# Kernel tuning notes

Hardware: AMD Instinct MI355X
Metric: run time of the kernel (lower is better)

## Reference

```python
import jax, jax.numpy as jnp
import numpy as np

TEMP = 0.5  # init kwarg `tmp`
NUM_CLASSES = 100


def setup_inputs() -> dict:
    key = jax.random.key(0)
    k1, k2 = jax.random.split(key)
    embedding = jax.random.normal(k1, (8192, 256), dtype=jnp.float32)
    label = jax.random.randint(k2, (8192,), 0, NUM_CLASSES, dtype=jnp.int64)
    return {"embedding": embedding, "label": label}


def reference(embedding, label):
    # Row-normalize -> pairwise cosine similarity [N, N]
    normed = embedding / jnp.linalg.norm(embedding, axis=1, keepdims=True)
    sim = (normed @ normed.T) / TEMP  # already divided by temperature

    N = embedding.shape[0]
    eye = jnp.eye(N, dtype=bool)

    # Denominator: sum of exp(sim) over off-diagonal entries per row
    exp_sim = jnp.exp(sim)
    row_sum = jnp.sum(jnp.where(eye, 0.0, exp_sim), axis=1)  # [N]

    # log(exp(sim_ij) / row_sum_i) = sim_ij - log(row_sum_i)
    log_prob = sim - jnp.log(row_sum)[:, None]

    # Positive mask: same label, i != j
    pos_mask = (label[:, None] == label[None, :]) & ~eye
    n_i = jnp.sum(pos_mask, axis=1)  # positives per anchor

    inner = jnp.sum(jnp.where(pos_mask, log_prob, 0.0), axis=1)  # [N]
    per_anchor = jnp.where(n_i > 0, -inner / jnp.maximum(n_i, 1).astype(sim.dtype), 0.0)
    return jnp.sum(per_anchor)
```

## Files before the change

kernel.cpp:

```cpp
#include <hip/hip_runtime.h>
#include <hip/hip_bf16.h>
#include <stdint.h>

#define N    8192
#define D    256
#define NCLS 100

static constexpr float TEMP    = 0.5f;
static constexpr float SCALE_F = 1.69864360f;
static constexpr float LN2     = 0.69314718055994531f;

#define NSLOT 130

typedef float f32x4 __attribute__((ext_vector_type(4)));

__device__ __forceinline__ unsigned short f2bf(float f) {
  union { float f; unsigned int u; } x; x.f = f;
  unsigned int r = x.u + 0x7fffu + ((x.u >> 16) & 1u);
  return (unsigned short)(r >> 16);
}
__device__ __forceinline__ float bf2f(unsigned short b) {
  union { unsigned int u; float f; } x; x.u = ((unsigned int)b) << 16;
  return x.f;
}


__global__ __launch_bounds__(256) void normalize_kernel(
    const float* __restrict__ emb, const long long* __restrict__ label,
    unsigned short* __restrict__ abf, unsigned char* __restrict__ a8,
    int* __restrict__ cnt, int* __restrict__ list) {
  const int row  = blockIdx.x * 4 + (threadIdx.x >> 6);
  const int lane = threadIdx.x & 63;
  const float4 v = ((const float4*)(emb + (size_t)row * D))[lane];
  float ss = v.x * v.x + v.y * v.y + v.z * v.z + v.w * v.w;
#pragma unroll
  for (int off = 1; off < 64; off <<= 1) ss += __shfl_xor(ss, off);
  const float s = rsqrtf(ss) * SCALE_F;
  const float x = v.x * s, y = v.y * s, z = v.z * s, wv = v.w * s;

  ushort4 o;
  o.x = f2bf(x); o.y = f2bf(y); o.z = f2bf(z); o.w = f2bf(wv);
  ((ushort4*)(abf + (size_t)row * D))[lane] = o;

  int p = __builtin_amdgcn_cvt_pk_fp8_f32(x, y, 0, false);
  p = __builtin_amdgcn_cvt_pk_fp8_f32(z, wv, p, true);
  *(int*)(a8 + (size_t)(row >> 4) * 4096 + (lane >> 1) * 128 +
          (row & 15) * 8 + (lane & 1) * 4) = p;

  if (lane == 0) {
    const int c = (int)label[row];
    const int slot = atomicAdd(cnt + c, 1);
    list[c * 256 + slot] = row;
  }
}

__global__ __launch_bounds__(256, 4) void simexp_rowsum_kernel(
    const unsigned char* __restrict__ A, float* __restrict__ part) {
  const int tid  = threadIdx.x;
  const int w    = tid >> 6;
  const int lane = tid & 63;
  const int quad = lane >> 4;
  const int l15  = lane & 15;

  const int b = blockIdx.x;
  int x = (int)((-1.0f + sqrtf(1.0f + 8.0f * (float)b)) * 0.5f);
  while ((x + 1) * (x + 2) / 2 <= b) ++x;
  while (x * (x + 1) / 2 > b) --x;
  const int y = b - x * (x + 1) / 2;

  const int row0 = y << 7;
  const int col0 = x << 7;
  const bool diag = (x == y);
  const int wm  = (w & 1) * 64;
  const int jn0 = (w >> 1) * 64;

  if (diag && wm > jn0) {
    part[((size_t)y * NSLOT + 2 * x + 0) * 128 + 64 + lane] = 0.f;
    part[((size_t)x * NSLOT + 128 + 1) * 128 + lane] = 0.f;
    return;
  }
  const bool needmask = diag && (wm == jn0);

  const unsigned char* Ap = A + (size_t)((row0 >> 4) + (w & 1) * 4) * 4096;
  const unsigned char* Bp = A + (size_t)((col0 >> 4) + (w >> 1) * 4) * 4096;

  f32x4 acc[4][4];
#pragma unroll
  for (int mt = 0; mt < 4; ++mt)
#pragma unroll
    for (int nt = 0; nt < 4; ++nt) acc[mt][nt] = (f32x4){0.f, 0.f, 0.f, 0.f};

#pragma unroll
  for (int kq = 0; kq < 4; ++kq) {
#pragma unroll
    for (int kkl = 0; kkl < 2; ++kkl) {
      const int fo = kq * 1024 + (kkl * 4 + quad) * 128 + l15 * 8;
      long af[4], bf[4];
#pragma unroll
      for (int mt = 0; mt < 4; ++mt)
        af[mt] = *(const long*)(Ap + mt * 4096 + fo);
#pragma unroll
      for (int nt = 0; nt < 4; ++nt)
        bf[nt] = *(const long*)(Bp + nt * 4096 + fo);
#pragma unroll
      for (int mt = 0; mt < 4; ++mt)
#pragma unroll
        for (int nt = 0; nt < 4; ++nt)
          acc[mt][nt] = __builtin_amdgcn_mfma_f32_16x16x32_fp8_fp8(
              af[mt], bf[nt], acc[mt][nt], 0, 0, 0);
    }
  }

  float rowpart[4][4];
  float colpart[4] = {0.f, 0.f, 0.f, 0.f};
#pragma unroll
  for (int mt = 0; mt < 4; ++mt)
#pragma unroll
    for (int e = 0; e < 4; ++e) rowpart[mt][e] = 0.f;
#pragma unroll
  for (int mt = 0; mt < 4; ++mt)
#pragma unroll
    for (int nt = 0; nt < 4; ++nt)
#pragma unroll
      for (int e = 0; e < 4; ++e) {
        float v = __builtin_amdgcn_exp2f(acc[mt][nt][e]);
        if (needmask) {
          const int iw = mt * 16 + quad * 4 + e;
          const int jw = nt * 16 + l15;
          v = (iw < jw) ? v : 0.f;
        }
        rowpart[mt][e] += v;
        colpart[nt] += v;
      }

  const int rslot = 2 * x + (jn0 >> 6);
  const int cslot = diag ? (128 + (wm >> 6)) : (2 * y + (wm >> 6));
  float* rowdst = part + ((size_t)y * NSLOT + rslot) * 128 + wm;
  float* coldst = part + ((size_t)x * NSLOT + cslot) * 128 + jn0;

#pragma unroll
  for (int nt = 0; nt < 4; ++nt) {
    float v = colpart[nt];
    v += __shfl_xor(v, 16);
    v += __shfl_xor(v, 32);
    if (quad == 0) coldst[nt * 16 + l15] = v;
  }
#pragma unroll
  for (int mt = 0; mt < 4; ++mt)
#pragma unroll
    for (int e = 0; e < 4; ++e) {
      float v = rowpart[mt][e];
      v += __shfl_xor(v, 1);
      v += __shfl_xor(v, 2);
      v += __shfl_xor(v, 4);
      v += __shfl_xor(v, 8);
      if (l15 == 0) rowdst[mt * 16 + quad * 4 + e] = v;
    }
}

__global__ __launch_bounds__(256) void finalize_kernel(
    const unsigned short* __restrict__ abf, const float* __restrict__ part,
    const long long* __restrict__ label, const int* __restrict__ cnt,
    const int* __restrict__ list, float* __restrict__ out) {
  __shared__ float red[4];
  __shared__ int rows_l[256];
  const int tid  = threadIdx.x;
  const int w    = tid >> 6;
  const int lane = tid & 63;

  if (blockIdx.x < NCLS) {
    const int c = blockIdx.x;
    const int m = cnt[c];
    if (m <= 1) return;
    if (tid < m) rows_l[tid] = list[c * 256 + tid];
    __syncthreads();
    float acc = 0.f;
    for (int s = 0; s < m; ++s)
      acc += bf2f(abf[(size_t)rows_l[s] * D + tid]);
    float v = acc * acc;
#pragma unroll
    for (int off = 1; off < 64; off <<= 1) v += __shfl_xor(v, off);
    if (lane == 0) red[w] = v;
    __syncthreads();
    if (tid == 0) {
      const float ssq = red[0] + red[1] + red[2] + red[3];
      const float term = (ssq * LN2 - 2.0f * (float)m) / (float)(m - 1);
      atomicAdd(out, -term);
    }
  } else {
    const int i = (blockIdx.x - NCLS) * 256 + tid;
    const int band = i >> 7, r = i & 127;
    const float* ps = part + (size_t)band * NSLOT * 128 + r;
    float rs = 0.f;
#pragma unroll 13
    for (int s = 0; s < NSLOT; ++s) rs += ps[(size_t)s * 128];
    const int c = (int)label[i];
    float v = 0.f;
    if (cnt[c] > 1)
      v = __builtin_amdgcn_logf(rs) * LN2;
#pragma unroll
    for (int off = 1; off < 64; off <<= 1) v += __shfl_xor(v, off);
    if (lane == 0) red[w] = v;
    __syncthreads();
    if (tid == 0)
      atomicAdd(out, red[0] + red[1] + red[2] + red[3]);
  }
}

extern "C" void kernel_launch(void* const* d_in, const int* in_sizes, int n_in,
                              void* d_out, int out_size, void* d_ws,
                              size_t ws_size, hipStream_t stream) {
  const float* emb = (const float*)d_in[0];
  const long long* label = (const long long*)d_in[1];
  float* out = (float*)d_out;

  char* ws = (char*)d_ws;
  unsigned short* abf = (unsigned short*)ws;
  unsigned char* a8 = (unsigned char*)(ws + (size_t)N * D * 2);
  float* part = (float*)(ws + (size_t)N * D * 3);
  int* cnt = (int*)(ws + (size_t)N * D * 3 + (size_t)64 * NSLOT * 128 * 4);
  int* list = cnt + 128;

  hipMemsetAsync(cnt, 0, 128 * 4, stream);
  hipMemsetAsync(out, 0, sizeof(float), stream);

  normalize_kernel<<<N / 4, 256, 0, stream>>>(emb, label, abf, a8, cnt, list);

  simexp_rowsum_kernel<<<2080, 256, 0, stream>>>(a8, part);

  finalize_kernel<<<NCLS + N / 256, 256, 0, stream>>>(abf, part, label, cnt,
                                                      list, out);
}
```

Baseline: 130.6 us.

## Stage FP8 A/B tiles in LDS via global_load_lds before MFMA loop

Each block now copies its 128x256 FP8 row and column tiles into shared memory with asynchronous global-to-LDS loads, then reads MFMA fragments from LDS instead of global memory. This removes duplicate global reads, since each fragment was previously fetched by two waves. It adds 64 KB of LDS per block, lowers the occupancy hint from 4 to 2 blocks, and inserts a barrier before compute. There is no overlap between the load and the compute.

```diff
diff --git a/kernel.cpp b/kernel.cpp
--- a/kernel.cpp
+++ b/kernel.cpp
@@ -22,6 +22,11 @@
 __device__ __forceinline__ float bf2f(unsigned short b) {
   union { unsigned int u; float f; } x; x.u = ((unsigned int)b) << 16;
   return x.f;
+}
+__device__ __forceinline__ void gld16(const void* g, void* l) {
+  __builtin_amdgcn_global_load_lds(
+      (const __attribute__((address_space(1))) unsigned int*)g,
+      (__attribute__((address_space(3))) unsigned int*)l, 16, 0, 0);
 }
 
 
@@ -54,8 +59,10 @@
   }
 }
 
-__global__ __launch_bounds__(256, 4) void simexp_rowsum_kernel(
+__global__ __launch_bounds__(256, 2) void simexp_rowsum_kernel(
     const unsigned char* __restrict__ A, float* __restrict__ part) {
+  __shared__ __align__(16) unsigned char sa[128 * 256];
+  __shared__ __align__(16) unsigned char sb[128 * 256];
   const int tid  = threadIdx.x;
   const int w    = tid >> 6;
   const int lane = tid & 63;
@@ -74,15 +81,26 @@
   const int wm  = (w & 1) * 64;
   const int jn0 = (w >> 1) * 64;
 
+#pragma unroll
+  for (int p = 0; p < 8; ++p) {
+    const int seg = w * 8 + p;
+    gld16(A + (size_t)((row0 >> 4) + (seg >> 2)) * 4096 + (seg & 3) * 1024 +
+              lane * 16,
+          sa + seg * 1024);
+    gld16(A + (size_t)((col0 >> 4) + (seg >> 2)) * 4096 + (seg & 3) * 1024 +
+              lane * 16,
+          sb + seg * 1024);
+  }
+  __syncthreads();
+
   if (diag && wm > jn0) {
-    part[((size_t)y * NSLOT + 2 * x + 0) * 128 + 64 + lane] = 0.f;
-    part[((size_t)x * NSLOT + 128 + 1) * 128 + lane] = 0.f;
+    part[((size_t)y * NSLOT + 2 * x) * 128 + 64 + lane] = 0.f;
+    part[((size_t)x * NSLOT + 129) * 128 + lane] = 0.f;
     return;
   }
   const bool needmask = diag && (wm == jn0);
-
-  const unsigned char* Ap = A + (size_t)((row0 >> 4) + (w & 1) * 4) * 4096;
-  const unsigned char* Bp = A + (size_t)((col0 >> 4) + (w >> 1) * 4) * 4096;
+  const int pam = (w & 1) * 4;
+  const int pbn = (w >> 1) * 4;
 
   f32x4 acc[4][4];
 #pragma unroll
@@ -98,10 +116,10 @@
       long af[4], bf[4];
 #pragma unroll
       for (int mt = 0; mt < 4; ++mt)
-        af[mt] = *(const long*)(Ap + mt * 4096 + fo);
+        af[mt] = *(const long*)(sa + (pam + mt) * 4096 + fo);
 #pragma unroll
       for (int nt = 0; nt < 4; ++nt)
-        bf[nt] = *(const long*)(Bp + nt * 4096 + fo);
+        bf[nt] = *(const long*)(sb + (pbn + nt) * 4096 + fo);
 #pragma unroll
       for (int mt = 0; mt < 4; ++mt)
 #pragma unroll
```

New measurement: 127.8 us. 2.2% less time.

## Interleave FP8 layout for 16-byte fragment loads and prefetch all operands upfront

Applied to the files above, without the earlier changes.

Changes the FP8 packed layout written by the normalize kernel so that each lane's two k-halves sit next to each other, which lets the GEMM kernel load 16 bytes per lane instead of 8. All A and B fragments are loaded into registers before the MFMA loop, so memory latency is exposed once rather than once per k-step. Launch bounds drop to 2 blocks per SM to leave room for the larger register footprint, which lowers occupancy.

```diff
diff --git a/kernel.cpp b/kernel.cpp
--- a/kernel.cpp
+++ b/kernel.cpp
@@ -13,6 +13,7 @@
 #define NSLOT 130
 
 typedef float f32x4 __attribute__((ext_vector_type(4)));
+typedef long  lx2  __attribute__((ext_vector_type(2)));
 
 __device__ __forceinline__ unsigned short f2bf(float f) {
   union { float f; unsigned int u; } x; x.f = f;
@@ -44,8 +45,9 @@
 
   int p = __builtin_amdgcn_cvt_pk_fp8_f32(x, y, 0, false);
   p = __builtin_amdgcn_cvt_pk_fp8_f32(z, wv, p, true);
-  *(int*)(a8 + (size_t)(row >> 4) * 4096 + (lane >> 1) * 128 +
-          (row & 15) * 8 + (lane & 1) * 4) = p;
+  *(int*)(a8 + (size_t)(row >> 4) * 4096 + (lane >> 4) * 1024 +
+          ((lane >> 1) & 3) * 256 + (row & 15) * 16 + ((lane >> 3) & 1) * 8 +
+          (lane & 1) * 4) = p;
 
   if (lane == 0) {
     const int c = (int)label[row];
@@ -54,7 +56,15 @@
   }
 }
 
-__global__ __launch_bounds__(256, 4) void simexp_rowsum_kernel(
+struct TileCoord { int x, y; };
+__device__ __forceinline__ TileCoord tri_decode(int b) {
+  int x = (int)((-1.0f + sqrtf(1.0f + 8.0f * (float)b)) * 0.5f);
+  while ((x + 1) * (x + 2) / 2 <= b) ++x;
+  while (x * (x + 1) / 2 > b) --x;
+  return {x, b - x * (x + 1) / 2};
+}
+
+__global__ __launch_bounds__(256, 2) void simexp_rowsum_kernel(
     const unsigned char* __restrict__ A, float* __restrict__ part) {
   const int tid  = threadIdx.x;
   const int w    = tid >> 6;
@@ -62,12 +72,8 @@
   const int quad = lane >> 4;
   const int l15  = lane & 15;
 
-  const int b = blockIdx.x;
-  int x = (int)((-1.0f + sqrtf(1.0f + 8.0f * (float)b)) * 0.5f);
-  while ((x + 1) * (x + 2) / 2 <= b) ++x;
-  while (x * (x + 1) / 2 > b) --x;
-  const int y = b - x * (x + 1) / 2;
-
+  const TileCoord tc = tri_decode(blockIdx.x);
+  const int x = tc.x, y = tc.y;
   const int row0 = y << 7;
   const int col0 = x << 7;
   const bool diag = (x == y);
@@ -75,14 +81,27 @@
   const int jn0 = (w >> 1) * 64;
 
   if (diag && wm > jn0) {
-    part[((size_t)y * NSLOT + 2 * x + 0) * 128 + 64 + lane] = 0.f;
-    part[((size_t)x * NSLOT + 128 + 1) * 128 + lane] = 0.f;
+    part[((size_t)y * NSLOT + 2 * x) * 128 + 64 + lane] = 0.f;
+    part[((size_t)x * NSLOT + 129) * 128 + lane] = 0.f;
     return;
   }
   const bool needmask = diag && (wm == jn0);
 
   const unsigned char* Ap = A + (size_t)((row0 >> 4) + (w & 1) * 4) * 4096;
   const unsigned char* Bp = A + (size_t)((col0 >> 4) + (w >> 1) * 4) * 4096;
+  const int lo = quad * 256 + l15 * 16;
+
+  lx2 aF[4][4], bF[4][4];
+#pragma unroll
+  for (int mt = 0; mt < 4; ++mt)
+#pragma unroll
+    for (int kq = 0; kq < 4; ++kq)
+      aF[mt][kq] = *(const lx2*)(Ap + mt * 4096 + kq * 1024 + lo);
+#pragma unroll
+  for (int nt = 0; nt < 4; ++nt)
+#pragma unroll
+    for (int kq = 0; kq < 4; ++kq)
+      bF[nt][kq] = *(const lx2*)(Bp + nt * 4096 + kq * 1024 + lo);
 
   f32x4 acc[4][4];
 #pragma unroll
@@ -91,25 +110,15 @@
     for (int nt = 0; nt < 4; ++nt) acc[mt][nt] = (f32x4){0.f, 0.f, 0.f, 0.f};
 
 #pragma unroll
-  for (int kq = 0; kq < 4; ++kq) {
-#pragma unroll
-    for (int kkl = 0; kkl < 2; ++kkl) {
-      const int fo = kq * 1024 + (kkl * 4 + quad) * 128 + l15 * 8;
-      long af[4], bf[4];
-#pragma unroll
-      for (int mt = 0; mt < 4; ++mt)
-        af[mt] = *(const long*)(Ap + mt * 4096 + fo);
-#pragma unroll
-      for (int nt = 0; nt < 4; ++nt)
-        bf[nt] = *(const long*)(Bp + nt * 4096 + fo);
+  for (int kq = 0; kq < 4; ++kq)
+#pragma unroll
+    for (int kkl = 0; kkl < 2; ++kkl)
 #pragma unroll
       for (int mt = 0; mt < 4; ++mt)
 #pragma unroll
         for (int nt = 0; nt < 4; ++nt)
           acc[mt][nt] = __builtin_amdgcn_mfma_f32_16x16x32_fp8_fp8(
-              af[mt], bf[nt], acc[mt][nt], 0, 0, 0);
-    }
-  }
+              aF[mt][kq][kkl], bF[nt][kq][kkl], acc[mt][nt], 0, 0, 0);
 
   float rowpart[4][4];
   float colpart[4] = {0.f, 0.f, 0.f, 0.f};
```

After: 122.6 us (median of 2 runs). 1.07x faster.
